# Performance work log

Measured on AMD Instinct MI355X. Metric: run time of the kernel, lower is better.

## Reference

```python
import jax, jax.numpy as jnp
import numpy as np

NUM_HEADS = 16


def setup_inputs() -> dict:
    key = jax.random.key(0)
    k1, k2, k3 = jax.random.split(key, 3)
    B, N, C = 8, 16384, 128  # window_size == dim == 128, N = ws*ws
    x = jax.random.normal(k1, (B, N, C), dtype=jnp.float32)
    w_qkv = jax.random.normal(k2, (3 * C, C), dtype=jnp.float32) * (C ** -0.5)
    b_qkv = jax.random.normal(k3, (3 * C,), dtype=jnp.float32) * 0.01
    return {"x": x, "w_qkv": w_qkv, "b_qkv": b_qkv}


def reference(x, w_qkv, b_qkv):
    B, N, C = x.shape
    ws = C  # the Linear over the last axis forces window_size == dim
    H = NUM_HEADS
    scale = (C // H) ** -0.5  # torch code scales by (dim//num_heads)**-0.5
    # [B,N,C] -> [B,ws,ws,C] -> [B,C,ws,ws]
    x4 = jnp.transpose(x.reshape(B, ws, ws, C), (0, 3, 1, 2))
    # Linear over last axis (length ws == dim): [B,C,ws,3C]
    qkv = jnp.einsum('bcwd,ed->bcwe', x4, w_qkv) + b_qkv
    # reshape(B,C,3,H,-1).permute(2,0,3,1,4) -> [3,B,H,C, ws*C/H]
    qkv = jnp.transpose(qkv.reshape(B, C, 3, H, -1), (2, 0, 3, 1, 4))
    q, k, v = qkv[0], qkv[1], qkv[2]  # each [B,H,C,D] with D = ws*C/H
    attn = jax.nn.softmax(jnp.einsum('bhcd,bhed->bhce', q, k) * scale, axis=-1)  # [B,H,C,C]
    out = jnp.einsum('bhce,bhed->bhcd', attn, v)  # [B,H,C,D]
    # transpose(1,2).reshape(B,C,ws,ws).permute(0,2,3,1).view(B,N,C)
    out = jnp.transpose(out, (0, 2, 1, 3)).reshape(B, C, ws, ws)
    out = jnp.transpose(out, (0, 2, 3, 1)).reshape(B, N, C)
    return out
```

## Files before the change

### kernel.cpp

```cpp
#include <hip/hip_runtime.h>
#include <hip/hip_bf16.h>
#include <stdint.h>


#define B_ 8
#define N_ 16384
#define C_ 128
#define H_ 16
#define E3 384
#define DH 1024

typedef float f32x4 __attribute__((ext_vector_type(4)));
typedef _Float16 f16x8 __attribute__((ext_vector_type(8)));
typedef unsigned short u16x8 __attribute__((ext_vector_type(8)));
typedef unsigned short u16x4 __attribute__((ext_vector_type(4)));

#define MFMA16(a, b, c) __builtin_amdgcn_mfma_f32_16x16x32_f16((a), (b), (c), 0, 0, 0)

__device__ __forceinline__ unsigned short f2h(float f) {
  union { _Float16 h; unsigned short u; } x;
  x.h = (_Float16)f;
  return x.u;
}

__global__ __launch_bounds__(256) void convert_w_kernel(const float* __restrict__ wq,
                                                        unsigned short* __restrict__ wh) {
  int i = blockIdx.x * 256 + threadIdx.x;
  float4 v = ((const float4*)wq)[i];
  u16x4 o;
  o[0] = f2h(v.x); o[1] = f2h(v.y); o[2] = f2h(v.z); o[3] = f2h(v.w);
  ((u16x4*)wh)[i] = o;
}

__global__ __launch_bounds__(256) void qkv_proj_kernel(
    const float* __restrict__ x,
    const float* __restrict__ wq,
    const unsigned short* __restrict__ wh,
    const float* __restrict__ bq,
    unsigned short* __restrict__ qk2,
    unsigned short* __restrict__ vT2) {
  const int w = blockIdx.x & 127;
  const int half = blockIdx.x >> 7;
  const int b = blockIdx.y;
  const int t = threadIdx.x;
  const int l = t & 63;
  const int wv = t >> 6;

  __shared__ __align__(16) unsigned short xt[128 * 128];
  char* xtb = (char*)xt;

  const float* xg = x + ((size_t)(b * N_ + w * 128)) * C_;
#pragma unroll
  for (int it = 0; it < 2; ++it) {
    int task = t + it * 256;
    int c0 = (task & 31) * 4;
    int d0 = (task >> 5) * 8;
    u16x8 pk0, pk1, pk2, pk3;
#pragma unroll
    for (int j = 0; j < 8; ++j) {
      float4 v = *(const float4*)(xg + (d0 + j) * C_ + c0);
      pk0[j] = f2h(v.x);
      pk1[j] = f2h(v.y);
      pk2[j] = f2h(v.z);
      pk3[j] = f2h(v.w);
    }
    *(u16x8*)(xtb + c0 * 256 + ((d0 * 2) ^ ((c0 & 7) << 4))) = pk0;
    *(u16x8*)(xtb + (c0 + 1) * 256 + ((d0 * 2) ^ (((c0 + 1) & 7) << 4))) = pk1;
    *(u16x8*)(xtb + (c0 + 2) * 256 + ((d0 * 2) ^ (((c0 + 2) & 7) << 4))) = pk2;
    *(u16x8*)(xtb + (c0 + 3) * 256 + ((d0 * 2) ^ (((c0 + 3) & 7) << 4))) = pk3;
  }
  __syncthreads();

  const int c00 = (wv & 1) * 64;
  const int ehalf = (wv >> 1) * 32;

  f16x8 ax[4][4];
#pragma unroll
  for (int mf = 0; mf < 4; ++mf)
#pragma unroll
    for (int ks = 0; ks < 4; ++ks) {
      int cl = c00 + mf * 16 + (l & 15);
      ax[mf][ks] = *(const f16x8*)(xtb + cl * 256 + (((ks * 64) + ((l >> 4) * 16)) ^ ((cl & 7) << 4)));
    }

  const f32x4 fzero = {0.f, 0.f, 0.f, 0.f};
  const bool useWh = (wh != nullptr);

#pragma unroll
  for (int es = 0; es < 3; ++es) {
    const int esub = half * 3 + es;
    const int e00 = esub * 64 + ehalf;
    const int f00 = w * E3 + e00;
    const int type = f00 >> 14;

    f16x8 bw[2][4];
#pragma unroll
    for (int nf = 0; nf < 2; ++nf)
#pragma unroll
      for (int ks = 0; ks < 4; ++ks) {
        int e = e00 + nf * 16 + (l & 15);
        if (useWh) {
          bw[nf][ks] = *(const f16x8*)(wh + e * 128 + ks * 32 + ((l >> 4) * 8));
        } else {
          const float* wp = wq + e * 128 + ks * 32 + ((l >> 4) * 8);
          float4 w0 = *(const float4*)(wp);
          float4 w1 = *(const float4*)(wp + 4);
          f16x8 bb;
          bb[0] = (_Float16)w0.x; bb[1] = (_Float16)w0.y;
          bb[2] = (_Float16)w0.z; bb[3] = (_Float16)w0.w;
          bb[4] = (_Float16)w1.x; bb[5] = (_Float16)w1.y;
          bb[6] = (_Float16)w1.z; bb[7] = (_Float16)w1.w;
          bw[nf][ks] = bb;
        }
      }

    f32x4 acc[4][2];
#pragma unroll
    for (int mf = 0; mf < 4; ++mf)
#pragma unroll
      for (int nf = 0; nf < 2; ++nf) acc[mf][nf] = fzero;

    if (type < 2) {
#pragma unroll
      for (int ks = 0; ks < 4; ++ks)
#pragma unroll
        for (int mf = 0; mf < 4; ++mf)
#pragma unroll
          for (int nf = 0; nf < 2; ++nf)
            acc[mf][nf] = MFMA16(bw[nf][ks], ax[mf][ks], acc[mf][nf]);
#pragma unroll
      for (int nf = 0; nf < 2; ++nf) {
        int ft = (f00 + nf * 16) >> 4;
        float4 bb = *(const float4*)(bq + e00 + nf * 16 + ((l >> 4) * 4));
#pragma unroll
        for (int mf = 0; mf < 4; ++mf) {
          int cb = (c00 >> 4) + mf;
          size_t tb = (((size_t)b * 2048 + ft) * 8 + cb) * 256;
          u16x4 ov;
          ov[0] = f2h(acc[mf][nf][0] + bb.x);
          ov[1] = f2h(acc[mf][nf][1] + bb.y);
          ov[2] = f2h(acc[mf][nf][2] + bb.z);
          ov[3] = f2h(acc[mf][nf][3] + bb.w);
          *(u16x4*)(qk2 + tb + l * 4) = ov;
        }
      }
    } else {
#pragma unroll
      for (int ks = 0; ks < 4; ++ks)
#pragma unroll
        for (int mf = 0; mf < 4; ++mf)
#pragma unroll
          for (int nf = 0; nf < 2; ++nf)
            acc[mf][nf] = MFMA16(ax[mf][ks], bw[nf][ks], acc[mf][nf]);
#pragma unroll
      for (int nf = 0; nf < 2; ++nf) {
        int fnf = f00 + nf * 16;
        int hh = (fnf >> 10) & 15;
        int ddt = (fnf & 1023) >> 4;
        float bias = bq[e00 + nf * 16 + (l & 15)];
#pragma unroll
        for (int mf = 0; mf < 4; ++mf) {
          int cb = (c00 >> 4) + mf;
          size_t tb = ((((size_t)b * 16 + hh) * 64 + ddt) * 8 + cb) * 256;
          u16x4 ov;
#pragma unroll
          for (int r = 0; r < 4; ++r) ov[r] = f2h(acc[mf][nf][r] + bias);
          *(u16x4*)(vT2 + tb + l * 4) = ov;
        }
      }
    }
  }
}

__global__ __launch_bounds__(256) void attn_kernel(
    const unsigned short* __restrict__ qk2,
    const unsigned short* __restrict__ vT2,
    float* __restrict__ out) {
  const int bid = blockIdx.x;
  const int ch = bid >> 7;
  const int bh = bid & 127;
  const int b = bh >> 4;
  const int h = bh & 15;
  const int t = threadIdx.x;
  const int l = t & 63;
  const int wv = t >> 6;

  __shared__ __align__(16) char smem[8192 + 32768 + 2048];
  char* QS = smem;
  char* KS = smem + 8192;
  float* RED = (float*)(smem + 40960);

  const f32x4 fzero = {0.f, 0.f, 0.f, 0.f};
  f32x4 acc[2][2];
#pragma unroll
  for (int mf = 0; mf < 2; ++mf)
#pragma unroll
    for (int nf = 0; nf < 2; ++nf) acc[mf][nf] = fzero;

  const int e0w = wv * 32;

  for (int dc = 0; dc < 8; ++dc) {
    const int ft0q = h * 64 + dc * 8;
    const int ft0k = 1024 + h * 64 + dc * 8;
#pragma unroll
    for (int i = 0; i < 2; ++i) {
      int idx = t + i * 256;
      int ftl = idx >> 6, cbl = (idx >> 5) & 1, m = idx & 31;
      int cb = ch * 2 + cbl;
      uint4 v = *(const uint4*)(qk2 + (((size_t)b * 2048 + ft0q + ftl) * 8 + cb) * 256 + m * 8);
      int row0 = cbl * 16 + (m & 7) * 2;
      int fb = ftl * 32 + (m >> 3) * 8;
      *(uint2*)(QS + row0 * 256 + (fb ^ ((row0 & 7) << 4))) = make_uint2(v.x, v.y);
      *(uint2*)(QS + (row0 + 1) * 256 + (fb ^ (((row0 + 1) & 7) << 4))) = make_uint2(v.z, v.w);
    }
#pragma unroll
    for (int i = 0; i < 8; ++i) {
      int idx = t + i * 256;
      int ftl = idx >> 8, cb = (idx >> 5) & 7, m = idx & 31;
      uint4 v = *(const uint4*)(qk2 + (((size_t)b * 2048 + ft0k + ftl) * 8 + cb) * 256 + m * 8);
      int row0 = cb * 16 + (m & 7) * 2;
      int fb = ftl * 32 + (m >> 3) * 8;
      *(uint2*)(KS + row0 * 256 + (fb ^ ((row0 & 7) << 4))) = make_uint2(v.x, v.y);
      *(uint2*)(KS + (row0 + 1) * 256 + (fb ^ (((row0 + 1) & 7) << 4))) = make_uint2(v.z, v.w);
    }
    __syncthreads();

#pragma unroll
    for (int ks = 0; ks < 4; ++ks) {
      f16x8 aQ[2], bK[2];
#pragma unroll
      for (int mf = 0; mf < 2; ++mf) {
        int cl = mf * 16 + (l & 15);
        aQ[mf] = *(const f16x8*)(QS + cl * 256 + (((ks * 64) + ((l >> 4) * 16)) ^ ((cl & 7) << 4)));
      }
#pragma unroll
      for (int nf = 0; nf < 2; ++nf) {
        int el = e0w + nf * 16 + (l & 15);
        bK[nf] = *(const f16x8*)(KS + el * 256 + (((ks * 64) + ((l >> 4) * 16)) ^ ((el & 7) << 4)));
      }
#pragma unroll
      for (int mf = 0; mf < 2; ++mf)
#pragma unroll
        for (int nf = 0; nf < 2; ++nf)
          acc[mf][nf] = MFMA16(aQ[mf], bK[nf], acc[mf][nf]);
    }
    __syncthreads();
  }

  const float SC = 0.35355339059327f * 1.44269504088896f;
  float mrow[2][4];
#pragma unroll
  for (int mf = 0; mf < 2; ++mf)
#pragma unroll
    for (int r = 0; r < 4; ++r) {
      float mx = fmaxf(acc[mf][0][r], acc[mf][1][r]);
      mx = fmaxf(mx, __shfl_xor(mx, 1));
      mx = fmaxf(mx, __shfl_xor(mx, 2));
      mx = fmaxf(mx, __shfl_xor(mx, 4));
      mx = fmaxf(mx, __shfl_xor(mx, 8));
      int cl = mf * 16 + ((l >> 4) * 4) + r;
      if ((l & 15) == 0) RED[cl * 4 + wv] = mx;
    }
  __syncthreads();
#pragma unroll
  for (int mf = 0; mf < 2; ++mf)
#pragma unroll
    for (int r = 0; r < 4; ++r) {
      int cl = mf * 16 + ((l >> 4) * 4) + r;
      float4 v = *(const float4*)(RED + cl * 4);
      mrow[mf][r] = fmaxf(fmaxf(v.x, v.y), fmaxf(v.z, v.w));
    }
#pragma unroll
  for (int mf = 0; mf < 2; ++mf)
#pragma unroll
    for (int r = 0; r < 4; ++r) {
      float s0 = 0.f;
#pragma unroll
      for (int nf = 0; nf < 2; ++nf) {
        float p = exp2f((acc[mf][nf][r] - mrow[mf][r]) * SC);
        acc[mf][nf][r] = p;
        s0 += p;
      }
      s0 += __shfl_xor(s0, 1);
      s0 += __shfl_xor(s0, 2);
      s0 += __shfl_xor(s0, 4);
      s0 += __shfl_xor(s0, 8);
      int cl = mf * 16 + ((l >> 4) * 4) + r;
      if ((l & 15) == 0) RED[256 + cl * 4 + wv] = s0;
    }
#pragma unroll
  for (int mf = 0; mf < 2; ++mf)
#pragma unroll
    for (int nf = 0; nf < 2; ++nf)
#pragma unroll
      for (int r = 0; r < 4; ++r) {
        int cl = mf * 16 + ((l >> 4) * 4) + r;
        int el = e0w + nf * 16 + (l & 15);
        *(unsigned short*)(QS + cl * 256 + ((el * 2) ^ ((cl & 7) << 4))) = f2h(acc[mf][nf][r]);
      }
  __syncthreads();
  float invc[2];
#pragma unroll
  for (int mf = 0; mf < 2; ++mf) {
    int cl = mf * 16 + (l & 15);
    float4 v = *(const float4*)(RED + 256 + cl * 4);
    invc[mf] = 1.f / (v.x + v.y + v.z + v.w);
  }

  for (int dc2 = 0; dc2 < 8; ++dc2) {
#pragma unroll
    for (int i = 0; i < 8; ++i) {
      int idx = t + i * 256;
      int ddtl = idx >> 8, cb = (idx >> 5) & 7, m = idx & 31;
      uint4 v = *(const uint4*)(vT2 + ((((size_t)(b * 16 + h)) * 64 + dc2 * 8 + ddtl) * 8 + cb) * 256 + m * 8);
      int row0 = ddtl * 16 + (m & 7) * 2;
      int cbyte = cb * 32 + (m >> 3) * 8;
      *(uint2*)(KS + row0 * 256 + (cbyte ^ ((row0 & 7) << 4))) = make_uint2(v.x, v.y);
      *(uint2*)(KS + (row0 + 1) * 256 + (cbyte ^ (((row0 + 1) & 7) << 4))) = make_uint2(v.z, v.w);
    }
    __syncthreads();

    f32x4 acc2[2][2];
#pragma unroll
    for (int nf = 0; nf < 2; ++nf)
#pragma unroll
      for (int mf = 0; mf < 2; ++mf) acc2[nf][mf] = fzero;

#pragma unroll
    for (int ks = 0; ks < 4; ++ks) {
      f16x8 aP[2], bV[2];
#pragma unroll
      for (int mf = 0; mf < 2; ++mf) {
        int cl = mf * 16 + (l & 15);
        aP[mf] = *(const f16x8*)(QS + cl * 256 + (((ks * 64) + ((l >> 4) * 16)) ^ ((cl & 7) << 4)));
      }
#pragma unroll
      for (int nf = 0; nf < 2; ++nf) {
        int dl = e0w + nf * 16 + (l & 15);
        bV[nf] = *(const f16x8*)(KS + dl * 256 + (((ks * 64) + ((l >> 4) * 16)) ^ ((dl & 7) << 4)));
      }
#pragma unroll
      for (int nf = 0; nf < 2; ++nf)
#pragma unroll
        for (int mf = 0; mf < 2; ++mf)
          acc2[nf][mf] = MFMA16(bV[nf], aP[mf], acc2[nf][mf]);
    }

#pragma unroll
    for (int nf = 0; nf < 2; ++nf)
#pragma unroll
      for (int mf = 0; mf < 2; ++mf) {
        int c = ch * 32 + mf * 16 + (l & 15);
#pragma unroll
        for (int r = 0; r < 4; ++r) {
          int d = dc2 * 128 + e0w + nf * 16 + ((l >> 4) * 4) + r;
          out[((size_t)(b * N_ + h * DH + d)) * C_ + c] = acc2[nf][mf][r] * invc[mf];
        }
      }
    __syncthreads();
  }
}

extern "C" void kernel_launch(void* const* d_in, const int* in_sizes, int n_in,
                              void* d_out, int out_size, void* d_ws, size_t ws_size,
                              hipStream_t stream) {
  const float* x = (const float*)d_in[0];
  const float* wq = (const float*)d_in[1];
  const float* bq = (const float*)d_in[2];
  unsigned short* qk2 = (unsigned short*)d_ws;
  unsigned short* vT2 = qk2 + 33554432UL;
  unsigned short* wh = vT2 + 16777216UL;

  const size_t baseNeed = (33554432UL + 16777216UL) * 2;
  if (ws_size < baseNeed) return;
  const bool useWh = ws_size >= baseNeed + 49152UL * 2;

  if (useWh) convert_w_kernel<<<48, 256, 0, stream>>>(wq, wh);
  qkv_proj_kernel<<<dim3(256, 8), 256, 0, stream>>>(x, wq, useWh ? wh : nullptr, bq, qk2, vT2);
  attn_kernel<<<512, 256, 0, stream>>>(qk2, vT2, (float*)d_out);
}
```

Baseline: 85.53 us.

## Software-pipeline global loads through registers in QKV projection and attention kernels

The projection kernel now handles two windows per block and prefetches the second window's x tile into registers while computing the first, which halves the grid. The attention kernel double-buffers its Q/K and V tile loads in registers, issuing the next chunk's global loads before the current chunk's MFMAs, and moves barriers to the top of the loop. The aim is to hide global memory latency behind compute, at the cost of more registers, possibly lower occupancy, and fewer blocks in the projection grid.

Result: slower. 95.99 us (+12.2%).

```diff
diff --git a/kernel.cpp b/kernel.cpp
--- a/kernel.cpp
+++ b/kernel.cpp
@@ -39,8 +39,8 @@
     const float* __restrict__ bq,
     unsigned short* __restrict__ qk2,
     unsigned short* __restrict__ vT2) {
-  const int w = blockIdx.x & 127;
-  const int half = blockIdx.x >> 7;
+  const int wp = blockIdx.x & 63;
+  const int half = blockIdx.x >> 6;
   const int b = blockIdx.y;
   const int t = threadIdx.x;
   const int l = t & 63;
@@ -49,7 +49,104 @@
   __shared__ __align__(16) unsigned short xt[128 * 128];
   char* xtb = (char*)xt;
 
-  const float* xg = x + ((size_t)(b * N_ + w * 128)) * C_;
+  const int w0 = wp * 2, w1 = w0 + 1;
+  const float* xg0 = x + ((size_t)(b * N_ + w0 * 128)) * C_;
+  const float* xg1 = xg0 + (size_t)128 * C_;
+
+  const int c00 = (wv & 1) * 64;
+  const int ehalf = (wv >> 1) * 32;
+  const f32x4 fzero = {0.f, 0.f, 0.f, 0.f};
+  const bool useWh = (wh != nullptr);
+
+  f16x8 ax[4][4];
+
+  auto compute_win = [&](int w) {
+#pragma unroll
+    for (int es = 0; es < 3; ++es) {
+      const int esub = half * 3 + es;
+      const int e00 = esub * 64 + ehalf;
+      const int f00 = w * E3 + e00;
+      const int type = f00 >> 14;
+
+      f16x8 bw[2][4];
+#pragma unroll
+      for (int nf = 0; nf < 2; ++nf)
+#pragma unroll
+        for (int ks = 0; ks < 4; ++ks) {
+          int e = e00 + nf * 16 + (l & 15);
+          if (useWh) {
+            bw[nf][ks] = *(const f16x8*)(wh + e * 128 + ks * 32 + ((l >> 4) * 8));
+          } else {
+            const float* wp_ = wq + e * 128 + ks * 32 + ((l >> 4) * 8);
+            float4 w0_ = *(const float4*)(wp_);
+            float4 w1_ = *(const float4*)(wp_ + 4);
+            f16x8 bb;
+            bb[0] = (_Float16)w0_.x; bb[1] = (_Float16)w0_.y;
+            bb[2] = (_Float16)w0_.z; bb[3] = (_Float16)w0_.w;
+            bb[4] = (_Float16)w1_.x; bb[5] = (_Float16)w1_.y;
+            bb[6] = (_Float16)w1_.z; bb[7] = (_Float16)w1_.w;
+            bw[nf][ks] = bb;
+          }
+        }
+
+      f32x4 acc[4][2];
+#pragma unroll
+      for (int mf = 0; mf < 4; ++mf)
+#pragma unroll
+        for (int nf = 0; nf < 2; ++nf) acc[mf][nf] = fzero;
+
+      if (type < 2) {
+#pragma unroll
+        for (int ks = 0; ks < 4; ++ks)
+#pragma unroll
+          for (int mf = 0; mf < 4; ++mf)
+#pragma unroll
+            for (int nf = 0; nf < 2; ++nf)
+              acc[mf][nf] = MFMA16(bw[nf][ks], ax[mf][ks], acc[mf][nf]);
+#pragma unroll
+        for (int nf = 0; nf < 2; ++nf) {
+          int ft = (f00 + nf * 16) >> 4;
+          float4 bb = *(const float4*)(bq + e00 + nf * 16 + ((l >> 4) * 4));
+#pragma unroll
+          for (int mf = 0; mf < 4; ++mf) {
+            int cb = (c00 >> 4) + mf;
+            size_t tb = (((size_t)b * 2048 + ft) * 8 + cb) * 256;
+            u16x4 ov;
+            ov[0] = f2h(acc[mf][nf][0] + bb.x);
+            ov[1] = f2h(acc[mf][nf][1] + bb.y);
+            ov[2] = f2h(acc[mf][nf][2] + bb.z);
+            ov[3] = f2h(acc[mf][nf][3] + bb.w);
+            *(u16x4*)(qk2 + tb + l * 4) = ov;
+          }
+        }
+      } else {
+#pragma unroll
+        for (int ks = 0; ks < 4; ++ks)
+#pragma unroll
+          for (int mf = 0; mf < 4; ++mf)
+#pragma unroll
+            for (int nf = 0; nf < 2; ++nf)
+              acc[mf][nf] = MFMA16(ax[mf][ks], bw[nf][ks], acc[mf][nf]);
+#pragma unroll
+        for (int nf = 0; nf < 2; ++nf) {
+          int fnf = f00 + nf * 16;
+          int hh = (fnf >> 10) & 15;
+          int ddt = (fnf & 1023) >> 4;
+          float bias = bq[e00 + nf * 16 + (l & 15)];
+#pragma unroll
+          for (int mf = 0; mf < 4; ++mf) {
+            int cb = (c00 >> 4) + mf;
+            size_t tb = ((((size_t)b * 16 + hh) * 64 + ddt) * 8 + cb) * 256;
+            u16x4 ov;
+#pragma unroll
+            for (int r = 0; r < 4; ++r) ov[r] = f2h(acc[mf][nf][r] + bias);
+            *(u16x4*)(vT2 + tb + l * 4) = ov;
+          }
+        }
+      }
+    }
+  };
+
 #pragma unroll
   for (int it = 0; it < 2; ++it) {
     int task = t + it * 256;
@@ -58,7 +155,7 @@
     u16x8 pk0, pk1, pk2, pk3;
 #pragma unroll
     for (int j = 0; j < 8; ++j) {
-      float4 v = *(const float4*)(xg + (d0 + j) * C_ + c0);
+      float4 v = *(const float4*)(xg0 + (d0 + j) * C_ + c0);
       pk0[j] = f2h(v.x);
       pk1[j] = f2h(v.y);
       pk2[j] = f2h(v.z);
@@ -71,10 +168,6 @@
   }
   __syncthreads();
 
-  const int c00 = (wv & 1) * 64;
-  const int ehalf = (wv >> 1) * 32;
-
-  f16x8 ax[4][4];
 #pragma unroll
   for (int mf = 0; mf < 4; ++mf)
 #pragma unroll
@@ -82,94 +175,51 @@
       int cl = c00 + mf * 16 + (l & 15);
       ax[mf][ks] = *(const f16x8*)(xtb + cl * 256 + (((ks * 64) + ((l >> 4) * 16)) ^ ((cl & 7) << 4)));
     }
-
-  const f32x4 fzero = {0.f, 0.f, 0.f, 0.f};
-  const bool useWh = (wh != nullptr);
-
-#pragma unroll
-  for (int es = 0; es < 3; ++es) {
-    const int esub = half * 3 + es;
-    const int e00 = esub * 64 + ehalf;
-    const int f00 = w * E3 + e00;
-    const int type = f00 >> 14;
-
-    f16x8 bw[2][4];
-#pragma unroll
-    for (int nf = 0; nf < 2; ++nf)
-#pragma unroll
-      for (int ks = 0; ks < 4; ++ks) {
-        int e = e00 + nf * 16 + (l & 15);
-        if (useWh) {
-          bw[nf][ks] = *(const f16x8*)(wh + e * 128 + ks * 32 + ((l >> 4) * 8));
-        } else {
-          const float* wp = wq + e * 128 + ks * 32 + ((l >> 4) * 8);
-          float4 w0 = *(const float4*)(wp);
-          float4 w1 = *(const float4*)(wp + 4);
-          f16x8 bb;
-          bb[0] = (_Float16)w0.x; bb[1] = (_Float16)w0.y;
-          bb[2] = (_Float16)w0.z; bb[3] = (_Float16)w0.w;
-          bb[4] = (_Float16)w1.x; bb[5] = (_Float16)w1.y;
-          bb[6] = (_Float16)w1.z; bb[7] = (_Float16)w1.w;
-          bw[nf][ks] = bb;
-        }
-      }
-
-    f32x4 acc[4][2];
-#pragma unroll
-    for (int mf = 0; mf < 4; ++mf)
-#pragma unroll
-      for (int nf = 0; nf < 2; ++nf) acc[mf][nf] = fzero;
-
-    if (type < 2) {
-#pragma unroll
-      for (int ks = 0; ks < 4; ++ks)
-#pragma unroll
-        for (int mf = 0; mf < 4; ++mf)
-#pragma unroll
-          for (int nf = 0; nf < 2; ++nf)
-            acc[mf][nf] = MFMA16(bw[nf][ks], ax[mf][ks], acc[mf][nf]);
-#pragma unroll
-      for (int nf = 0; nf < 2; ++nf) {
-        int ft = (f00 + nf * 16) >> 4;
-        float4 bb = *(const float4*)(bq + e00 + nf * 16 + ((l >> 4) * 4));
-#pragma unroll
-        for (int mf = 0; mf < 4; ++mf) {
-          int cb = (c00 >> 4) + mf;
-          size_t tb = (((size_t)b * 2048 + ft) * 8 + cb) * 256;
-          u16x4 ov;
-          ov[0] = f2h(acc[mf][nf][0] + bb.x);
-          ov[1] = f2h(acc[mf][nf][1] + bb.y);
-          ov[2] = f2h(acc[mf][nf][2] + bb.z);
-          ov[3] = f2h(acc[mf][nf][3] + bb.w);
-          *(u16x4*)(qk2 + tb + l * 4) = ov;
-        }
-      }
-    } else {
-#pragma unroll
-      for (int ks = 0; ks < 4; ++ks)
-#pragma unroll
-        for (int mf = 0; mf < 4; ++mf)
-#pragma unroll
-          for (int nf = 0; nf < 2; ++nf)
-            acc[mf][nf] = MFMA16(ax[mf][ks], bw[nf][ks], acc[mf][nf]);
-#pragma unroll
-      for (int nf = 0; nf < 2; ++nf) {
-        int fnf = f00 + nf * 16;
-        int hh = (fnf >> 10) & 15;
-        int ddt = (fnf & 1023) >> 4;
-        float bias = bq[e00 + nf * 16 + (l & 15)];
-#pragma unroll
-        for (int mf = 0; mf < 4; ++mf) {
-          int cb = (c00 >> 4) + mf;
-          size_t tb = ((((size_t)b * 16 + hh) * 64 + ddt) * 8 + cb) * 256;
-          u16x4 ov;
-#pragma unroll
-          for (int r = 0; r < 4; ++r) ov[r] = f2h(acc[mf][nf][r] + bias);
-          *(u16x4*)(vT2 + tb + l * 4) = ov;
-        }
-      }
-    }
-  }
+  __syncthreads();
+
+  float4 st[16];
+#pragma unroll
+  for (int it = 0; it < 2; ++it) {
+    int task = t + it * 256;
+    int c0 = (task & 31) * 4;
+    int d0 = (task >> 5) * 8;
+#pragma unroll
+    for (int j = 0; j < 8; ++j)
+      st[it * 8 + j] = *(const float4*)(xg1 + (d0 + j) * C_ + c0);
+  }
+
+  compute_win(w0);
+
+#pragma unroll
+  for (int it = 0; it < 2; ++it) {
+    int task = t + it * 256;
+    int c0 = (task & 31) * 4;
+    int d0 = (task >> 5) * 8;
+    u16x8 pk0, pk1, pk2, pk3;
+#pragma unroll
+    for (int j = 0; j < 8; ++j) {
+      float4 v = st[it * 8 + j];
+      pk0[j] = f2h(v.x);
+      pk1[j] = f2h(v.y);
+      pk2[j] = f2h(v.z);
+      pk3[j] = f2h(v.w);
+    }
+    *(u16x8*)(xtb + c0 * 256 + ((d0 * 2) ^ ((c0 & 7) << 4))) = pk0;
+    *(u16x8*)(xtb + (c0 + 1) * 256 + ((d0 * 2) ^ (((c0 + 1) & 7) << 4))) = pk1;
+    *(u16x8*)(xtb + (c0 + 2) * 256 + ((d0 * 2) ^ (((c0 + 2) & 7) << 4))) = pk2;
+    *(u16x8*)(xtb + (c0 + 3) * 256 + ((d0 * 2) ^ (((c0 + 3) & 7) << 4))) = pk3;
+  }
+  __syncthreads();
+
+#pragma unroll
+  for (int mf = 0; mf < 4; ++mf)
+#pragma unroll
+    for (int ks = 0; ks < 4; ++ks) {
+      int cl = c00 + mf * 16 + (l & 15);
+      ax[mf][ks] = *(const f16x8*)(xtb + cl * 256 + (((ks * 64) + ((l >> 4) * 16)) ^ ((cl & 7) << 4)));
+    }
+
+  compute_win(w1);
 }
 
 __global__ __launch_bounds__(256) void attn_kernel(
@@ -199,31 +249,64 @@
 
   const int e0w = wv * 32;
 
-  for (int dc = 0; dc < 8; ++dc) {
-    const int ft0q = h * 64 + dc * 8;
-    const int ft0k = 1024 + h * 64 + dc * 8;
+  uint4 qv[2], kv[8];
+  {
+    const int ft0q = h * 64;
+    const int ft0k = 1024 + h * 64;
 #pragma unroll
     for (int i = 0; i < 2; ++i) {
       int idx = t + i * 256;
       int ftl = idx >> 6, cbl = (idx >> 5) & 1, m = idx & 31;
-      int cb = ch * 2 + cbl;
-      uint4 v = *(const uint4*)(qk2 + (((size_t)b * 2048 + ft0q + ftl) * 8 + cb) * 256 + m * 8);
-      int row0 = cbl * 16 + (m & 7) * 2;
-      int fb = ftl * 32 + (m >> 3) * 8;
-      *(uint2*)(QS + row0 * 256 + (fb ^ ((row0 & 7) << 4))) = make_uint2(v.x, v.y);
-      *(uint2*)(QS + (row0 + 1) * 256 + (fb ^ (((row0 + 1) & 7) << 4))) = make_uint2(v.z, v.w);
+      qv[i] = *(const uint4*)(qk2 + (((size_t)b * 2048 + ft0q + ftl) * 8 + ch * 2 + cbl) * 256 + m * 8);
     }
 #pragma unroll
     for (int i = 0; i < 8; ++i) {
       int idx = t + i * 256;
       int ftl = idx >> 8, cb = (idx >> 5) & 7, m = idx & 31;
-      uint4 v = *(const uint4*)(qk2 + (((size_t)b * 2048 + ft0k + ftl) * 8 + cb) * 256 + m * 8);
+      kv[i] = *(const uint4*)(qk2 + (((size_t)b * 2048 + ft0k + ftl) * 8 + cb) * 256 + m * 8);
+    }
+  }
+
+  for (int dc = 0; dc < 8; ++dc) {
+    if (dc) __syncthreads();
+#pragma unroll
+    for (int i = 0; i < 2; ++i) {
+      int idx = t + i * 256;
+      int ftl = idx >> 6, cbl = (idx >> 5) & 1, m = idx & 31;
+      int row0 = cbl * 16 + (m & 7) * 2;
+      int fb = ftl * 32 + (m >> 3) * 8;
+      uint4 v = qv[i];
+      *(uint2*)(QS + row0 * 256 + (fb ^ ((row0 & 7) << 4))) = make_uint2(v.x, v.y);
+      *(uint2*)(QS + (row0 + 1) * 256 + (fb ^ (((row0 + 1) & 7) << 4))) = make_uint2(v.z, v.w);
+    }
+#pragma unroll
+    for (int i = 0; i < 8; ++i) {
+      int idx = t + i * 256;
+      int ftl = idx >> 8, cb = (idx >> 5) & 7, m = idx & 31;
       int row0 = cb * 16 + (m & 7) * 2;
       int fb = ftl * 32 + (m >> 3) * 8;
+      uint4 v = kv[i];
       *(uint2*)(KS + row0 * 256 + (fb ^ ((row0 & 7) << 4))) = make_uint2(v.x, v.y);
       *(uint2*)(KS + (row0 + 1) * 256 + (fb ^ (((row0 + 1) & 7) << 4))) = make_uint2(v.z, v.w);
     }
     __syncthreads();
+
+    if (dc < 7) {
+      const int ft0q = h * 64 + (dc + 1) * 8;
+      const int ft0k = 1024 + h * 64 + (dc + 1) * 8;
+#pragma unroll
+      for (int i = 0; i < 2; ++i) {
+        int idx = t + i * 256;
+        int ftl = idx >> 6, cbl = (idx >> 5) & 1, m = idx & 31;
+        qv[i] = *(const uint4*)(qk2 + (((size_t)b * 2048 + ft0q + ftl) * 8 + ch * 2 + cbl) * 256 + m * 8);
+      }
+#pragma unroll
+      for (int i = 0; i < 8; ++i) {
+        int idx = t + i * 256;
+        int ftl = idx >> 8, cb = (idx >> 5) & 7, m = idx & 31;
+        kv[i] = *(const uint4*)(qk2 + (((size_t)b * 2048 + ft0k + ftl) * 8 + cb) * 256 + m * 8);
+      }
+    }
 
 #pragma unroll
     for (int ks = 0; ks < 4; ++ks) {
@@ -244,7 +327,14 @@
         for (int nf = 0; nf < 2; ++nf)
           acc[mf][nf] = MFMA16(aQ[mf], bK[nf], acc[mf][nf]);
     }
-    __syncthreads();
+  }
+
+  uint4 vv[8];
+#pragma unroll
+  for (int i = 0; i < 8; ++i) {
+    int idx = t + i * 256;
+    int ddtl = idx >> 8, cb = (idx >> 5) & 7, m = idx & 31;
+    vv[i] = *(const uint4*)(vT2 + ((((size_t)(b * 16 + h)) * 64 + ddtl) * 8 + cb) * 256 + m * 8);
   }
 
   const float SC = 0.35355339059327f * 1.44269504088896f;
@@ -308,17 +398,27 @@
   }
 
   for (int dc2 = 0; dc2 < 8; ++dc2) {
+    if (dc2) __syncthreads();
 #pragma unroll
     for (int i = 0; i < 8; ++i) {
       int idx = t + i * 256;
       int ddtl = idx >> 8, cb = (idx >> 5) & 7, m = idx & 31;
-      uint4 v = *(const uint4*)(vT2 + ((((size_t)(b * 16 + h)) * 64 + dc2 * 8 + ddtl) * 8 + cb) * 256 + m * 8);
       int row0 = ddtl * 16 + (m & 7) * 2;
       int cbyte = cb * 32 + (m >> 3) * 8;
+      uint4 v = vv[i];
       *(uint2*)(KS + row0 * 256 + (cbyte ^ ((row0 & 7) << 4))) = make_uint2(v.x, v.y);
       *(uint2*)(KS + (row0 + 1) * 256 + (cbyte ^ (((row0 + 1) & 7) << 4))) = make_uint2(v.z, v.w);
     }
     __syncthreads();
+
+    if (dc2 < 7) {
+#pragma unroll
+      for (int i = 0; i < 8; ++i) {
+        int idx = t + i * 256;
+        int ddtl = idx >> 8, cb = (idx >> 5) & 7, m = idx & 31;
+        vv[i] = *(const uint4*)(vT2 + ((((size_t)(b * 16 + h)) * 64 + (dc2 + 1) * 8 + ddtl) * 8 + cb) * 256 + m * 8);
+      }
+    }
 
     f32x4 acc2[2][2];
 #pragma unroll
@@ -357,7 +457,6 @@
           out[((size_t)(b * N_ + h * DH + d)) * C_ + c] = acc2[nf][mf][r] * invc[mf];
         }
       }
-    __syncthreads();
   }
 }
 
@@ -376,6 +475,6 @@
   const bool useWh = ws_size >= baseNeed + 49152UL * 2;
 
   if (useWh) convert_w_kernel<<<48, 256, 0, stream>>>(wq, wh);
-  qkv_proj_kernel<<<dim3(256, 8), 256, 0, stream>>>(x, wq, useWh ? wh : nullptr, bq, qk2, vT2);
+  qkv_proj_kernel<<<dim3(128, 8), 256, 0, stream>>>(x, wq, useWh ? wh : nullptr, bq, qk2, vT2);
   attn_kernel<<<512, 256, 0, stream>>>(qk2, vT2, (float*)d_out);
 }
```

## Register-prefetch next Q/K/V tiles in attention loops and use nontemporal stores

Applied to the files above, without the earlier changes.

The attention kernel now loads the next chunk of Q/K (and later V) from global memory into registers while the current chunk is processed with MFMA. This hides global load latency behind compute instead of stalling at each loop start, and moves the barriers to the top of each iteration. The QKV projection writes its fp16 outputs with nontemporal stores to reduce cache pollution. The prefetch buffers add register pressure, which may lower occupancy.

Measured after the change: 90.66 us. 1.06x slower.

```diff
diff --git a/kernel.cpp b/kernel.cpp
--- a/kernel.cpp
+++ b/kernel.cpp
@@ -21,6 +21,12 @@
   union { _Float16 h; unsigned short u; } x;
   x.h = (_Float16)f;
   return x.u;
+}
+
+__device__ __forceinline__ void nt_store8(unsigned short* p, u16x4 v) {
+  union { u16x4 v; unsigned long long u; } cv;
+  cv.v = v;
+  __builtin_nontemporal_store(cv.u, (unsigned long long*)p);
 }
 
 __global__ __launch_bounds__(256) void convert_w_kernel(const float* __restrict__ wq,
@@ -141,7 +147,7 @@
           ov[1] = f2h(acc[mf][nf][1] + bb.y);
           ov[2] = f2h(acc[mf][nf][2] + bb.z);
           ov[3] = f2h(acc[mf][nf][3] + bb.w);
-          *(u16x4*)(qk2 + tb + l * 4) = ov;
+          nt_store8(qk2 + tb + l * 4, ov);
         }
       }
     } else {
@@ -165,7 +171,7 @@
           u16x4 ov;
 #pragma unroll
           for (int r = 0; r < 4; ++r) ov[r] = f2h(acc[mf][nf][r] + bias);
-          *(u16x4*)(vT2 + tb + l * 4) = ov;
+          nt_store8(vT2 + tb + l * 4, ov);
         }
       }
     }
@@ -199,31 +205,64 @@
 
   const int e0w = wv * 32;
 
-  for (int dc = 0; dc < 8; ++dc) {
-    const int ft0q = h * 64 + dc * 8;
-    const int ft0k = 1024 + h * 64 + dc * 8;
+  uint4 qv[2], kv[8];
+  {
+    const int ft0q = h * 64;
+    const int ft0k = 1024 + h * 64;
 #pragma unroll
     for (int i = 0; i < 2; ++i) {
       int idx = t + i * 256;
       int ftl = idx >> 6, cbl = (idx >> 5) & 1, m = idx & 31;
-      int cb = ch * 2 + cbl;
-      uint4 v = *(const uint4*)(qk2 + (((size_t)b * 2048 + ft0q + ftl) * 8 + cb) * 256 + m * 8);
-      int row0 = cbl * 16 + (m & 7) * 2;
-      int fb = ftl * 32 + (m >> 3) * 8;
-      *(uint2*)(QS + row0 * 256 + (fb ^ ((row0 & 7) << 4))) = make_uint2(v.x, v.y);
-      *(uint2*)(QS + (row0 + 1) * 256 + (fb ^ (((row0 + 1) & 7) << 4))) = make_uint2(v.z, v.w);
+      qv[i] = *(const uint4*)(qk2 + (((size_t)b * 2048 + ft0q + ftl) * 8 + ch * 2 + cbl) * 256 + m * 8);
     }
 #pragma unroll
     for (int i = 0; i < 8; ++i) {
       int idx = t + i * 256;
       int ftl = idx >> 8, cb = (idx >> 5) & 7, m = idx & 31;
-      uint4 v = *(const uint4*)(qk2 + (((size_t)b * 2048 + ft0k + ftl) * 8 + cb) * 256 + m * 8);
+      kv[i] = *(const uint4*)(qk2 + (((size_t)b * 2048 + ft0k + ftl) * 8 + cb) * 256 + m * 8);
+    }
+  }
+
+  for (int dc = 0; dc < 8; ++dc) {
+    if (dc) __syncthreads();
+#pragma unroll
+    for (int i = 0; i < 2; ++i) {
+      int idx = t + i * 256;
+      int ftl = idx >> 6, cbl = (idx >> 5) & 1, m = idx & 31;
+      int row0 = cbl * 16 + (m & 7) * 2;
+      int fb = ftl * 32 + (m >> 3) * 8;
+      uint4 v = qv[i];
+      *(uint2*)(QS + row0 * 256 + (fb ^ ((row0 & 7) << 4))) = make_uint2(v.x, v.y);
+      *(uint2*)(QS + (row0 + 1) * 256 + (fb ^ (((row0 + 1) & 7) << 4))) = make_uint2(v.z, v.w);
+    }
+#pragma unroll
+    for (int i = 0; i < 8; ++i) {
+      int idx = t + i * 256;
+      int ftl = idx >> 8, cb = (idx >> 5) & 7, m = idx & 31;
       int row0 = cb * 16 + (m & 7) * 2;
       int fb = ftl * 32 + (m >> 3) * 8;
+      uint4 v = kv[i];
       *(uint2*)(KS + row0 * 256 + (fb ^ ((row0 & 7) << 4))) = make_uint2(v.x, v.y);
       *(uint2*)(KS + (row0 + 1) * 256 + (fb ^ (((row0 + 1) & 7) << 4))) = make_uint2(v.z, v.w);
     }
     __syncthreads();
+
+    if (dc < 7) {
+      const int ft0q = h * 64 + (dc + 1) * 8;
+      const int ft0k = 1024 + h * 64 + (dc + 1) * 8;
+#pragma unroll
+      for (int i = 0; i < 2; ++i) {
+        int idx = t + i * 256;
+        int ftl = idx >> 6, cbl = (idx >> 5) & 1, m = idx & 31;
+        qv[i] = *(const uint4*)(qk2 + (((size_t)b * 2048 + ft0q + ftl) * 8 + ch * 2 + cbl) * 256 + m * 8);
+      }
+#pragma unroll
+      for (int i = 0; i < 8; ++i) {
+        int idx = t + i * 256;
+        int ftl = idx >> 8, cb = (idx >> 5) & 7, m = idx & 31;
+        kv[i] = *(const uint4*)(qk2 + (((size_t)b * 2048 + ft0k + ftl) * 8 + cb) * 256 + m * 8);
+      }
+    }
 
 #pragma unroll
     for (int ks = 0; ks < 4; ++ks) {
@@ -244,7 +283,14 @@
         for (int nf = 0; nf < 2; ++nf)
           acc[mf][nf] = MFMA16(aQ[mf], bK[nf], acc[mf][nf]);
     }
-    __syncthreads();
+  }
+
+  uint4 vv[8];
+#pragma unroll
+  for (int i = 0; i < 8; ++i) {
+    int idx = t + i * 256;
+    int ddtl = idx >> 8, cb = (idx >> 5) & 7, m = idx & 31;
+    vv[i] = *(const uint4*)(vT2 + ((((size_t)(b * 16 + h)) * 64 + ddtl) * 8 + cb) * 256 + m * 8);
   }
 
   const float SC = 0.35355339059327f * 1.44269504088896f;
@@ -308,17 +354,27 @@
   }
 
   for (int dc2 = 0; dc2 < 8; ++dc2) {
+    if (dc2) __syncthreads();
 #pragma unroll
     for (int i = 0; i < 8; ++i) {
       int idx = t + i * 256;
       int ddtl = idx >> 8, cb = (idx >> 5) & 7, m = idx & 31;
-      uint4 v = *(const uint4*)(vT2 + ((((size_t)(b * 16 + h)) * 64 + dc2 * 8 + ddtl) * 8 + cb) * 256 + m * 8);
       int row0 = ddtl * 16 + (m & 7) * 2;
       int cbyte = cb * 32 + (m >> 3) * 8;
+      uint4 v = vv[i];
       *(uint2*)(KS + row0 * 256 + (cbyte ^ ((row0 & 7) << 4))) = make_uint2(v.x, v.y);
       *(uint2*)(KS + (row0 + 1) * 256 + (cbyte ^ (((row0 + 1) & 7) << 4))) = make_uint2(v.z, v.w);
     }
     __syncthreads();
+
+    if (dc2 < 7) {
+#pragma unroll
+      for (int i = 0; i < 8; ++i) {
+        int idx = t + i * 256;
+        int ddtl = idx >> 8, cb = (idx >> 5) & 7, m = idx & 31;
+        vv[i] = *(const uint4*)(vT2 + ((((size_t)(b * 16 + h)) * 64 + (dc2 + 1) * 8 + ddtl) * 8 + cb) * 256 + m * 8);
+      }
+    }
 
     f32x4 acc2[2][2];
 #pragma unroll
@@ -357,7 +413,6 @@
           out[((size_t)(b * N_ + h * DH + d)) * C_ + c] = acc2[nf][mf][r] * invc[mf];
         }
       }
-    __syncthreads();
   }
 }
 
```
